# Performance work log

Hardware: AMD Instinct MI355X
Metric: run time of the kernel (lower is better)

## Reference

```python
import jax, jax.numpy as jnp
import numpy as np

B, S, E, HID, NH = 32, 512, 512, 512, 8
HD = E // NH  # head dim
A1, A2 = 1024, 1024  # architecture
EPS = 1e-5


def layer_norm(x, g, b):
    mu = jnp.mean(x, axis=-1, keepdims=True)
    var = jnp.mean(jnp.square(x - mu), axis=-1, keepdims=True)
    return (x - mu) * jax.lax.rsqrt(var + EPS) * g + b


def setup_inputs() -> dict:
    key = jax.random.key(0)
    ks = jax.random.split(key, 16)
    w = lambda k, shp: (jax.random.normal(k, shp, dtype=jnp.float32) * 0.02)
    return {
        'x': jax.random.normal(ks[0], (B, S, E), dtype=jnp.float32),
        'in_proj_w': w(ks[1], (3 * E, E)),
        'in_proj_b': jnp.zeros((3 * E,), jnp.float32),
        'out_proj_w': w(ks[2], (E, E)),
        'out_proj_b': jnp.zeros((E,), jnp.float32),
        'ln_g': jnp.ones((HID,), jnp.float32),
        'ln_b': jnp.zeros((HID,), jnp.float32),
        'w_ih': w(ks[3], (4 * HID, E)),
        'w_hh': w(ks[4], (4 * HID, HID)),
        'b_ih': jnp.zeros((4 * HID,), jnp.float32),
        'b_hh': jnp.zeros((4 * HID,), jnp.float32),
        'fc_w1': w(ks[5], (A1, HID)),
        'fc_b1': jnp.zeros((A1,), jnp.float32),
        'fc_w2': w(ks[6], (A2, A1)),
        'fc_b2': jnp.zeros((A2,), jnp.float32),
        'fc_wo': w(ks[7], (HID, A2)),
        'fc_bo': jnp.zeros((HID,), jnp.float32),
    }


def reference(x, in_proj_w, in_proj_b, out_proj_w, out_proj_b, ln_g, ln_b,
              w_ih, w_hh, b_ih, b_hh, fc_w1, fc_b1, fc_w2, fc_b2, fc_wo, fc_bo):
    # --- MultiheadAttention (self-attention, batch_first) ---
    qkv = x @ in_proj_w.T + in_proj_b            # [B,S,3E]
    q, k, v = jnp.split(qkv, 3, axis=-1)
    q = q.reshape(B, S, NH, HD)
    k = k.reshape(B, S, NH, HD)
    v = v.reshape(B, S, NH, HD)
    scores = jnp.einsum('bqhd,bkhd->bhqk', q, k) / np.float32(np.sqrt(HD))
    attn = jax.nn.softmax(scores, axis=-1)
    ctx = jnp.einsum('bhqk,bkhd->bqhd', attn, v).reshape(B, S, E)
    attn_out = ctx @ out_proj_w.T + out_proj_b
    attn_out = layer_norm(attn_out + x, ln_g, ln_b)  # [B,S,E]

    # --- LSTMCell unrolled over time via scan ---
    def step(carry, xt):
        hn, cn = carry
        gates = xt @ w_ih.T + b_ih + hn @ w_hh.T + b_hh  # [B,4H]
        i, f, g, o = jnp.split(gates, 4, axis=-1)
        i = jax.nn.sigmoid(i); f = jax.nn.sigmoid(f)
        g = jnp.tanh(g);       o = jax.nn.sigmoid(o)
        cn = f * cn + i * g
        hn = o * jnp.tanh(cn)
        return (hn, cn), hn

    h0 = jnp.zeros((B, HID), jnp.float32)
    c0 = jnp.zeros((B, HID), jnp.float32)
    (hn, cn), hs = jax.lax.scan(step, (h0, c0), attn_out.transpose(1, 0, 2))
    hs = hs.transpose(1, 0, 2)                   # [B,S,HID]

    # --- DeepNeuralNetwork MLP (applied pointwise over timesteps) ---
    h1 = jax.nn.relu(hs @ fc_w1.T + fc_b1)
    h2 = jax.nn.relu(h1 @ fc_w2.T + fc_b2)
    out = h2 @ fc_wo.T + fc_bo                   # [B,S,HID]

    out = layer_norm(out + attn_out, ln_g, ln_b)
    return out, (hn, cn)
```

## Files before the change

### kernel.cpp

```cpp
#include <hip/hip_runtime.h>

#define B_ 32
#define S_ 512
#define E_ 512
#define BS_ (B_*S_)

typedef __bf16 bf16x8 __attribute__((ext_vector_type(8)));
typedef float f32x4 __attribute__((ext_vector_type(4)));
typedef unsigned short u16x8 __attribute__((ext_vector_type(8)));

__device__ __forceinline__ unsigned short f2bf(float f){
  unsigned u = __float_as_uint(f);
  u += 0x7fffu + ((u>>16)&1u);
  return (unsigned short)(u>>16);
}
__device__ __forceinline__ float bf2f(unsigned short u){
  return __uint_as_float(((unsigned)u)<<16);
}
__device__ __forceinline__ float sigm(float x){ return 1.f/(1.f+__expf(-x)); }
__device__ __forceinline__ float tanh_f(float x){
  x = fminf(fmaxf(x,-15.f),15.f);
  float t=__expf(2.f*x); return (t-1.f)/(t+1.f);
}
__device__ __forceinline__ void gload_lds16(const void* g, void* l){
  __builtin_amdgcn_global_load_lds((const __attribute__((address_space(1))) unsigned int*)g,
                                   (__attribute__((address_space(3))) unsigned int*)l, 16, 0, 0);
}

__global__ void cast_bf16_k(const float* __restrict__ in, unsigned short* __restrict__ out, int n4){
  int i = blockIdx.x*256 + threadIdx.x;
  if (i < n4){
    const float4 v = *(const float4*)(in + (size_t)i*4);
    ushort4 o; o.x=f2bf(v.x); o.y=f2bf(v.y); o.z=f2bf(v.z); o.w=f2bf(v.w);
    *(ushort4*)(out + (size_t)i*4) = o;
  }
}
__global__ void addb_k(const float* __restrict__ a, const float* __restrict__ b, float* __restrict__ o, int n){
  int i = blockIdx.x*256 + threadIdx.x;
  if (i < n) o[i] = a[i] + b[i];
}
__global__ void sentinel_k(float* __restrict__ o){ o[0] = 1e9f; }

template<int OUTF , bool RELU>
__global__ __launch_bounds__(256) void gemm_bt(const unsigned short* __restrict__ A,
    const unsigned short* __restrict__ Bw, const float* __restrict__ bias,
    void* __restrict__ Cout, int M, int N, int K){
  __shared__ unsigned short As[128*32];
  __shared__ unsigned short Bs[128*32];
  const int tid = threadIdx.x, lane = tid&63, wid = tid>>6;
  const int bm = blockIdx.y, bn = blockIdx.x;
  const int wr = wid>>1, wc = wid&1;
  const int r = lane&15, kq = lane>>4;
  f32x4 acc[4][4] = {};
  const int nkt = K>>5;
  for (int kt=0; kt<nkt; ++kt){
#pragma unroll
    for (int i=0;i<2;++i){
      int cid = i*256 + tid;
      int row = cid>>2, kc = cid&3;
      int gcol = (kt<<5) + kc*8;
      gload_lds16(A  + (size_t)(bm*128+row)*K + gcol, (char*)As + (i*256 + wid*64)*16);
      gload_lds16(Bw + (size_t)(bn*128+row)*K + gcol, (char*)Bs + (i*256 + wid*64)*16);
    }
    __syncthreads();
    bf16x8 af[4], bfr[4];
#pragma unroll
    for (int i=0;i<4;++i){
      af[i]  = *(const bf16x8*)(As + (wr*64 + i*16 + r)*32 + kq*8);
      bfr[i] = *(const bf16x8*)(Bs + (wc*64 + i*16 + r)*32 + kq*8);
    }
#pragma unroll
    for (int i=0;i<4;++i)
#pragma unroll
      for (int j=0;j<4;++j)
        acc[i][j] = __builtin_amdgcn_mfma_f32_16x16x32_bf16(af[i], bfr[j], acc[i][j], 0,0,0);
    __syncthreads();
  }
#pragma unroll
  for (int j=0;j<4;++j){
    int n = bn*128 + wc*64 + j*16 + r;
    float bv = bias[n];
#pragma unroll
    for (int i=0;i<4;++i){
      int m0 = bm*128 + wr*64 + i*16 + kq*4;
#pragma unroll
      for (int jj=0;jj<4;++jj){
        float v = acc[i][j][jj] + bv;
        if (RELU) v = fmaxf(v, 0.f);
        size_t idx = (size_t)(m0+jj)*N + n;
        if (OUTF==0) ((unsigned short*)Cout)[idx] = f2bf(v);
        else         ((float*)Cout)[idx] = v;
      }
    }
  }
}

__global__ __launch_bounds__(256) void attn_k(const unsigned short* __restrict__ qkv,
                                              unsigned short* __restrict__ ctx){
  __shared__ unsigned short Qs[128*64];
  __shared__ unsigned short Ks[128*64];
  __shared__ unsigned short Vt[64*128];
  __shared__ unsigned short Ps[128*128];
  const int tid=threadIdx.x, lane=tid&63, wid=tid>>6;
  const int qt=blockIdx.x, bh=blockIdx.y, b=bh>>3, h=bh&7;
  const int r=lane&15, kq=lane>>4;
  const int q0=qt*128;
#pragma unroll
  for (int i=0;i<4;++i){
    int cid=i*256+tid; int row=cid>>3, dc=cid&7;
    u16x8 v = *(const u16x8*)(qkv + (size_t)(b*S_+q0+row)*1536 + h*64 + dc*8);
    int byte = (row*128 + dc*16) ^ ((row&7)<<4);
    *(u16x8*)((char*)Qs + byte) = v;
  }
  float m_run[2][4], l_run[2][4];
  f32x4 o_acc[2][4] = {};
#pragma unroll
  for (int a=0;a<2;++a)
#pragma unroll
    for (int j=0;j<4;++j){ m_run[a][j]=-1e30f; l_run[a][j]=0.f; }
  for (int kt=0; kt<4; ++kt){
#pragma unroll
    for (int i=0;i<4;++i){
      int cid=i*256+tid; int row=cid>>3, dc=cid&7;
      u16x8 v = *(const u16x8*)(qkv + (size_t)(b*S_+kt*128+row)*1536 + 512 + h*64 + dc*8);
      int byte = (row*128 + dc*16) ^ ((row&7)<<4);
      *(u16x8*)((char*)Ks + byte) = v;
    }
#pragma unroll
    for (int i=0;i<4;++i){
      int cid=i*256+tid; int sv=cid>>3, dc=cid&7;
      u16x8 v = *(const u16x8*)(qkv + (size_t)(b*S_+kt*128+sv)*1536 + 1024 + h*64 + dc*8);
#pragma unroll
      for (int e=0;e<8;++e){
        int d=dc*8+e;
        int byte = (d*256 + sv*2) ^ ((d&7)<<4);
        *(unsigned short*)((char*)Vt + byte) = (unsigned short)v[e];
      }
    }
    __syncthreads();
    f32x4 sa[2][8] = {};
#pragma unroll
    for (int dstep=0; dstep<2; ++dstep){
      int d0 = dstep*32 + kq*8;
      int q1 = wid*32 + r, q2 = wid*32 + 16 + r;
      bf16x8 a0 = *(const bf16x8*)((char*)Qs + ((q1*128 + d0*2) ^ ((q1&7)<<4)));
      bf16x8 a1 = *(const bf16x8*)((char*)Qs + ((q2*128 + d0*2) ^ ((q2&7)<<4)));
#pragma unroll
      for (int fk=0; fk<8; ++fk){
        int kc = fk*16 + r;
        bf16x8 bk = *(const bf16x8*)((char*)Ks + ((kc*128 + d0*2) ^ ((kc&7)<<4)));
        sa[0][fk] = __builtin_amdgcn_mfma_f32_16x16x32_bf16(a0, bk, sa[0][fk],0,0,0);
        sa[1][fk] = __builtin_amdgcn_mfma_f32_16x16x32_bf16(a1, bk, sa[1][fk],0,0,0);
      }
    }
#pragma unroll
    for (int fq=0; fq<2; ++fq){
#pragma unroll
      for (int j=0;j<4;++j){
        float mx = -1e30f;
#pragma unroll
        for (int fk=0;fk<8;++fk) mx = fmaxf(mx, sa[fq][fk][j]);
        mx *= 0.125f;
#pragma unroll
        for (int off=1; off<16; off<<=1) mx = fmaxf(mx, __shfl_xor(mx, off));
        float mn = fmaxf(m_run[fq][j], mx);
        float corr = __expf(m_run[fq][j] - mn);
        float ps = 0.f;
#pragma unroll
        for (int fk=0;fk<8;++fk){
          float p = __expf(sa[fq][fk][j]*0.125f - mn);
          sa[fq][fk][j] = p; ps += p;
        }
#pragma unroll
        for (int off=1; off<16; off<<=1) ps += __shfl_xor(ps, off);
        l_run[fq][j] = l_run[fq][j]*corr + ps;
        m_run[fq][j] = mn;
#pragma unroll
        for (int fd=0; fd<4; ++fd) o_acc[fq][fd][j] *= corr;
      }
    }
#pragma unroll
    for (int fq=0;fq<2;++fq)
#pragma unroll
      for (int fk=0;fk<8;++fk)
#pragma unroll
        for (int j=0;j<4;++j){
          int qr = wid*32 + fq*16 + kq*4 + j;
          int kc = fk*16 + r;
          int byte = (qr*256 + kc*2) ^ ((qr&7)<<4);
          *(unsigned short*)((char*)Ps + byte) = f2bf(sa[fq][fk][j]);
        }
#pragma unroll
    for (int kk=0;kk<4;++kk){
      int k0 = kk*32 + kq*8;
      bf16x8 pa[2];
#pragma unroll
      for (int fq=0;fq<2;++fq){
        int q = wid*32 + fq*16 + r;
        pa[fq] = *(const bf16x8*)((char*)Ps + ((q*256 + k0*2) ^ ((q&7)<<4)));
      }
#pragma unroll
      for (int fd=0; fd<4; ++fd){
        int d = fd*16 + r;
        bf16x8 bv = *(const bf16x8*)((char*)Vt + ((d*256 + k0*2) ^ ((d&7)<<4)));
        o_acc[0][fd] = __builtin_amdgcn_mfma_f32_16x16x32_bf16(pa[0], bv, o_acc[0][fd],0,0,0);
        o_acc[1][fd] = __builtin_amdgcn_mfma_f32_16x16x32_bf16(pa[1], bv, o_acc[1][fd],0,0,0);
      }
    }
    __syncthreads();
  }
#pragma unroll
  for (int fq=0;fq<2;++fq)
#pragma unroll
    for (int fd=0;fd<4;++fd)
#pragma unroll
      for (int j=0;j<4;++j){
        int qr = q0 + wid*32 + fq*16 + kq*4 + j;
        float v = o_acc[fq][fd][j] / l_run[fq][j];
        ctx[(size_t)(b*S_+qr)*512 + h*64 + fd*16 + r] = f2bf(v);
      }
}

template<bool DUAL>
__global__ __launch_bounds__(64) void ln_k(const float* __restrict__ raw, const float* __restrict__ res,
    const float* __restrict__ gam, const float* __restrict__ bet,
    float* __restrict__ outf, unsigned short* __restrict__ outb){
  const int row=blockIdx.x, lane=threadIdx.x;
  const size_t base=(size_t)row*512 + lane*8;
  float v[8];
  {
    float4 a0=*(const float4*)(raw+base), a1=*(const float4*)(raw+base+4);
    float4 b0=*(const float4*)(res+base), b1=*(const float4*)(res+base+4);
    v[0]=a0.x+b0.x; v[1]=a0.y+b0.y; v[2]=a0.z+b0.z; v[3]=a0.w+b0.w;
    v[4]=a1.x+b1.x; v[5]=a1.y+b1.y; v[6]=a1.z+b1.z; v[7]=a1.w+b1.w;
  }
  float s=0.f;
#pragma unroll
  for (int k=0;k<8;++k) s+=v[k];
#pragma unroll
  for (int off=1;off<64;off<<=1) s+=__shfl_xor(s,off);
  float mu=s*(1.f/512.f);
  float q=0.f;
#pragma unroll
  for (int k=0;k<8;++k){ float d=v[k]-mu; q+=d*d; }
#pragma unroll
  for (int off=1;off<64;off<<=1) q+=__shfl_xor(q,off);
  float rs=rsqrtf(q*(1.f/512.f)+1e-5f);
  float gv[8], bv[8];
  *(float4*)gv=*(const float4*)(gam+lane*8); *(float4*)(gv+4)=*(const float4*)(gam+lane*8+4);
  *(float4*)bv=*(const float4*)(bet+lane*8); *(float4*)(bv+4)=*(const float4*)(bet+lane*8+4);
  float y[8];
#pragma unroll
  for (int k=0;k<8;++k) y[k]=(v[k]-mu)*rs*gv[k]+bv[k];
  *(float4*)(outf+base)   = make_float4(y[0],y[1],y[2],y[3]);
  *(float4*)(outf+base+4) = make_float4(y[4],y[5],y[6],y[7]);
  if (DUAL){
    u16x8 ob;
#pragma unroll
    for (int k=0;k<8;++k) ob[k]=f2bf(y[k]);
    int row2 = ((row&511)<<5) | (row>>9);
    *(u16x8*)(outb + (size_t)row2*512 + lane*8)=ob;
  }
}

__global__ __launch_bounds__(256,1) void lstm_tag_k(
    const unsigned short* __restrict__ whh,
    const unsigned short* __restrict__ xpart,
    unsigned short* __restrict__ hs,
    float* __restrict__ hn_out, float* __restrict__ cn_out,
    unsigned* __restrict__ hxch)
{
  __shared__ unsigned short Wsl[64*512];
  __shared__ unsigned short Hb[32*512];
  const int tid=threadIdx.x, lane=tid&63, wid=tid>>6;
  const int wg=blockIdx.x;
  const int r=lane&15, kq=lane>>4;
  const int c=r, gate=c&3, uo=(wid<<2)+(c>>2), unit=wg*16+uo;
  const int colL=wid*16+c;
#pragma unroll
  for (int i=0;i<16;++i){
    int ch=i*256+tid; int lc=ch>>6, kc=ch&63;
    int uoo=((lc>>4)<<2)+((lc&15)>>2), gg=lc&3;
    u16x8 v = *(const u16x8*)(whh + (size_t)(gg*512 + wg*16 + uoo)*512 + kc*8);
    int byte=(lc*1024+kc*16)^((lc&7)<<4);
    *(u16x8*)((char*)Wsl+byte)=v;
  }
  {
    f32x4 z={0.f,0.f,0.f,0.f};
#pragma unroll
    for (int i=0;i<8;++i)
      *(f32x4*)((char*)Hb + (i*256+tid)*16) = z;
  }
  const int gb=tid>>3, gc=tid&7;
  float cst[8]={0,0,0,0,0,0,0,0}, hlast[8]={0,0,0,0,0,0,0,0};
  float xpc[8];
#pragma unroll
  for (int s=0;s<8;++s){
    int bb=(s>>2)*16 + kq*4 + (s&3);
    xpc[s]=bf2f(xpart[(size_t)bb*2048 + gate*512 + unit]);
  }
  __syncthreads();
  for (int t=0;t<512;++t){
    if (t){
      const unsigned* gp = hxch + (size_t)((t-1)&1)*16384 + gb*512 + gc*64;
      uint4 w0,w1,w2,w3,w4,w5,w6,w7,w8,w9,wa,wb,wc_,wd,we,wf;
      const unsigned tg=(unsigned)t;
      int it=0;
      for(;;){
        asm volatile(
          "global_load_dwordx4 %0, %16, off sc0 sc1\n\t"
          "global_load_dwordx4 %1, %16, off offset:16 sc0 sc1\n\t"
          "global_load_dwordx4 %2, %16, off offset:32 sc0 sc1\n\t"
          "global_load_dwordx4 %3, %16, off offset:48 sc0 sc1\n\t"
          "global_load_dwordx4 %4, %16, off offset:64 sc0 sc1\n\t"
          "global_load_dwordx4 %5, %16, off offset:80 sc0 sc1\n\t"
          "global_load_dwordx4 %6, %16, off offset:96 sc0 sc1\n\t"
          "global_load_dwordx4 %7, %16, off offset:112 sc0 sc1\n\t"
          "global_load_dwordx4 %8, %16, off offset:128 sc0 sc1\n\t"
          "global_load_dwordx4 %9, %16, off offset:144 sc0 sc1\n\t"
          "global_load_dwordx4 %10, %16, off offset:160 sc0 sc1\n\t"
          "global_load_dwordx4 %11, %16, off offset:176 sc0 sc1\n\t"
          "global_load_dwordx4 %12, %16, off offset:192 sc0 sc1\n\t"
          "global_load_dwordx4 %13, %16, off offset:208 sc0 sc1\n\t"
          "global_load_dwordx4 %14, %16, off offset:224 sc0 sc1\n\t"
          "global_load_dwordx4 %15, %16, off offset:240 sc0 sc1\n\t"
          "s_waitcnt vmcnt(0)"
          : "=&v"(w0),"=&v"(w1),"=&v"(w2),"=&v"(w3),"=&v"(w4),"=&v"(w5),"=&v"(w6),"=&v"(w7),
            "=&v"(w8),"=&v"(w9),"=&v"(wa),"=&v"(wb),"=&v"(wc_),"=&v"(wd),"=&v"(we),"=&v"(wf)
          : "v"(gp) : "memory");
        bool ok =
          ((w0.x&0xffffu)==tg)&((w0.y&0xffffu)==tg)&((w0.z&0xffffu)==tg)&((w0.w&0xffffu)==tg)&
          ((w1.x&0xffffu)==tg)&((w1.y&0xffffu)==tg)&((w1.z&0xffffu)==tg)&((w1.w&0xffffu)==tg)&
          ((w2.x&0xffffu)==tg)&((w2.y&0xffffu)==tg)&((w2.z&0xffffu)==tg)&((w2.w&0xffffu)==tg)&
          ((w3.x&0xffffu)==tg)&((w3.y&0xffffu)==tg)&((w3.z&0xffffu)==tg)&((w3.w&0xffffu)==tg)&
          ((w4.x&0xffffu)==tg)&((w4.y&0xffffu)==tg)&((w4.z&0xffffu)==tg)&((w4.w&0xffffu)==tg)&
          ((w5.x&0xffffu)==tg)&((w5.y&0xffffu)==tg)&((w5.z&0xffffu)==tg)&((w5.w&0xffffu)==tg)&
          ((w6.x&0xffffu)==tg)&((w6.y&0xffffu)==tg)&((w6.z&0xffffu)==tg)&((w6.w&0xffffu)==tg)&
          ((w7.x&0xffffu)==tg)&((w7.y&0xffffu)==tg)&((w7.z&0xffffu)==tg)&((w7.w&0xffffu)==tg)&
          ((w8.x&0xffffu)==tg)&((w8.y&0xffffu)==tg)&((w8.z&0xffffu)==tg)&((w8.w&0xffffu)==tg)&
          ((w9.x&0xffffu)==tg)&((w9.y&0xffffu)==tg)&((w9.z&0xffffu)==tg)&((w9.w&0xffffu)==tg)&
          ((wa.x&0xffffu)==tg)&((wa.y&0xffffu)==tg)&((wa.z&0xffffu)==tg)&((wa.w&0xffffu)==tg)&
          ((wb.x&0xffffu)==tg)&((wb.y&0xffffu)==tg)&((wb.z&0xffffu)==tg)&((wb.w&0xffffu)==tg)&
          ((wc_.x&0xffffu)==tg)&((wc_.y&0xffffu)==tg)&((wc_.z&0xffffu)==tg)&((wc_.w&0xffffu)==tg)&
          ((wd.x&0xffffu)==tg)&((wd.y&0xffffu)==tg)&((wd.z&0xffffu)==tg)&((wd.w&0xffffu)==tg)&
          ((we.x&0xffffu)==tg)&((we.y&0xffffu)==tg)&((we.z&0xffffu)==tg)&((we.w&0xffffu)==tg)&
          ((wf.x&0xffffu)==tg)&((wf.y&0xffffu)==tg)&((wf.z&0xffffu)==tg)&((wf.w&0xffffu)==tg);
        if (ok) break;
        if (++it>65536) break;
      }
      const int base = gb*1024 + gc*128;
      const int swz = (gb&7)<<4;
#define PACK2(WA,WB,G) { \
        uint4 p; \
        p.x=(WA.x>>16)|(WA.y&0xffff0000u); p.y=(WA.z>>16)|(WA.w&0xffff0000u); \
        p.z=(WB.x>>16)|(WB.y&0xffff0000u); p.w=(WB.z>>16)|(WB.w&0xffff0000u); \
        *(uint4*)((char*)Hb + ((base + (G)*16)^swz)) = p; }
      PACK2(w0,w1,0) PACK2(w2,w3,1) PACK2(w4,w5,2) PACK2(w6,w7,3)
      PACK2(w8,w9,4) PACK2(wa,wb,5) PACK2(wc_,wd,6) PACK2(we,wf,7)
#undef PACK2
    }
    __syncthreads();
    f32x4 acc[2];
    acc[0][0]=xpc[0]; acc[0][1]=xpc[1]; acc[0][2]=xpc[2]; acc[0][3]=xpc[3];
    acc[1][0]=xpc[4]; acc[1][1]=xpc[5]; acc[1][2]=xpc[6]; acc[1][3]=xpc[7];
#pragma unroll
    for (int ki=0;ki<16;++ki){
      int kb=ki*64+kq*16;
      bf16x8 a0=*(const bf16x8*)((char*)Hb+((r*1024+kb)^((r&7)<<4)));
      bf16x8 a1=*(const bf16x8*)((char*)Hb+(((16+r)*1024+kb)^((r&7)<<4)));
      bf16x8 bw=*(const bf16x8*)((char*)Wsl+((colL*1024+kb)^((colL&7)<<4)));
      acc[0]=__builtin_amdgcn_mfma_f32_16x16x32_bf16(a0,bw,acc[0],0,0,0);
      acc[1]=__builtin_amdgcn_mfma_f32_16x16x32_bf16(a1,bw,acc[1],0,0,0);
    }
    float xpn[8]={0,0,0,0,0,0,0,0};
    if (t<511){
#pragma unroll
      for (int s=0;s<8;++s){
        int bb=(s>>2)*16 + kq*4 + (s&3);
        xpn[s]=bf2f(xpart[(size_t)((t+1)*32+bb)*2048 + gate*512 + unit]);
      }
    }
    unsigned* pb = hxch + (size_t)(t&1)*16384;
#pragma unroll
    for (int s=0;s<8;++s){
      float v=acc[s>>2][s&3];
      float n1=__shfl_xor(v,1), n2=__shfl_xor(v,2), n3=__shfl_xor(v,3);
      if (gate==0){
        int bb=(s>>2)*16 + kq*4 + (s&3);
        float ig=sigm(v), fg=sigm(n1), gg2=tanh_f(n2), og=sigm(n3);
        float cn=fg*cst[s]+ig*gg2; cst[s]=cn;
        float hn=og*tanh_f(cn); hlast[s]=hn;
        unsigned h16=(unsigned)f2bf(hn);
        hs[((size_t)bb*512+t)*512 + unit]=(unsigned short)h16;
        unsigned word=(h16<<16)|(unsigned)(t+1);
        unsigned long long ad=(unsigned long long)(pb + bb*512 + unit);
        asm volatile("global_store_dword %0, %1, off sc0 sc1" :: "v"(ad), "v"(word) : "memory");
      }
    }
#pragma unroll
    for (int s=0;s<8;++s) xpc[s]=xpn[s];
    __syncthreads();
  }
  if (gate==0){
#pragma unroll
    for (int s=0;s<8;++s){
      int bb=(s>>2)*16 + kq*4 + (s&3);
      hn_out[(size_t)bb*512+unit]=hlast[s];
      cn_out[(size_t)bb*512+unit]=cst[s];
    }
  }
}

extern "C" void kernel_launch(void* const* d_in, const int* in_sizes, int n_in,
                              void* d_out, int out_size, void* d_ws, size_t ws_size,
                              hipStream_t stream) {
  const float* x          =(const float*)d_in[0];
  const float* in_proj_w  =(const float*)d_in[1];
  const float* in_proj_b  =(const float*)d_in[2];
  const float* out_proj_w =(const float*)d_in[3];
  const float* out_proj_b =(const float*)d_in[4];
  const float* ln_g       =(const float*)d_in[5];
  const float* ln_b       =(const float*)d_in[6];
  const float* w_ih       =(const float*)d_in[7];
  const float* w_hh       =(const float*)d_in[8];
  const float* b_ih       =(const float*)d_in[9];
  const float* b_hh       =(const float*)d_in[10];
  const float* fc_w1      =(const float*)d_in[11];
  const float* fc_b1      =(const float*)d_in[12];
  const float* fc_w2      =(const float*)d_in[13];
  const float* fc_b2      =(const float*)d_in[14];
  const float* fc_wo      =(const float*)d_in[15];
  const float* fc_bo      =(const float*)d_in[16];

  size_t off=0;
  auto A=[&](size_t b)->char*{ char* p=(char*)d_ws+off; off+=(b+255)&~(size_t)255; return p; };
  unsigned short* wqkv =(unsigned short*)A((size_t)1536*512*2);
  unsigned short* wout =(unsigned short*)A((size_t)512*512*2);
  unsigned short* wih  =(unsigned short*)A((size_t)2048*512*2);
  unsigned short* whh  =(unsigned short*)A((size_t)2048*512*2);
  unsigned short* w1   =(unsigned short*)A((size_t)1024*512*2);
  unsigned short* w2   =(unsigned short*)A((size_t)1024*1024*2);
  unsigned short* wo   =(unsigned short*)A((size_t)512*1024*2);
  float*          biasc=(float*)A(2048*4);
  unsigned*       hxch =(unsigned*)A((size_t)2*32*512*4);
  char* regA = A((size_t)BS_*512*2);
  char* regB = A((size_t)BS_*2048*2);
  char* regC = A((size_t)BS_*512*4);
  if (off > ws_size){ sentinel_k<<<1,1,0,stream>>>((float*)d_out); return; }

  unsigned short* xb        =(unsigned short*)regA;
  unsigned short* attn_outb =(unsigned short*)regA;
  unsigned short* hs        =(unsigned short*)regA;
  unsigned short* qkvb      =(unsigned short*)regB;
  unsigned short* ctxb      =(unsigned short*)(regB + (size_t)BS_*1536*2);
  unsigned short* xpart     =(unsigned short*)regB;
  unsigned short* h1b       =(unsigned short*)regB;
  unsigned short* h2b       =(unsigned short*)(regB + (size_t)BS_*1024*2);
  float*          attn_out  =(float*)regC;
  float* outp  =(float*)d_out;
  float* attn_raw = outp;
  float* out_raw  = outp;
  float* hn_out=outp + (size_t)BS_*512;
  float* cn_out=hn_out + (size_t)B_*512;

  auto cast=[&](const float* in, unsigned short* out, size_t n){
    int n4=(int)(n/4);
    cast_bf16_k<<<(n4+255)/256,256,0,stream>>>(in,out,n4);
  };
  cast(x, xb, (size_t)BS_*512);
  cast(in_proj_w, wqkv, (size_t)1536*512);
  cast(out_proj_w, wout, (size_t)512*512);
  cast(w_ih, wih, (size_t)2048*512);
  cast(w_hh, whh, (size_t)2048*512);
  cast(fc_w1, w1, (size_t)1024*512);
  cast(fc_w2, w2, (size_t)1024*1024);
  cast(fc_wo, wo, (size_t)512*1024);
  addb_k<<<8,256,0,stream>>>(b_ih,b_hh,biasc,2048);
  hipMemsetAsync(hxch,0,(size_t)2*32*512*4,stream);

  gemm_bt<0,false><<<dim3(12,128),256,0,stream>>>(xb,wqkv,in_proj_b,qkvb,BS_,1536,512);
  attn_k<<<dim3(4,256),256,0,stream>>>(qkvb,ctxb);
  gemm_bt<1,false><<<dim3(4,128),256,0,stream>>>(ctxb,wout,out_proj_b,attn_raw,BS_,512,512);
  ln_k<true><<<BS_,64,0,stream>>>(attn_raw,x,ln_g,ln_b,attn_out,attn_outb);
  gemm_bt<0,false><<<dim3(16,128),256,0,stream>>>(attn_outb,wih,biasc,xpart,BS_,2048,512);
  lstm_tag_k<<<32,256,0,stream>>>(whh,xpart,hs,hn_out,cn_out,hxch);
  gemm_bt<0,true><<<dim3(8,128),256,0,stream>>>(hs,w1,fc_b1,h1b,BS_,1024,512);
  gemm_bt<0,true><<<dim3(8,128),256,0,stream>>>(h1b,w2,fc_b2,h2b,BS_,1024,1024);
  gemm_bt<1,false><<<dim3(4,128),256,0,stream>>>(h2b,wo,fc_bo,out_raw,BS_,512,1024);
  ln_k<false><<<BS_,64,0,stream>>>(out_raw,attn_out,ln_g,ln_b,outp,nullptr);
}
```

Before: 4.225 ms.

## Replicate LSTM h-exchange per XCD, double-buffer LDS h, drop trailing barrier

Each block reads its XCD ID from a hardware register and polls a per-XCD replica of the hidden-state exchange buffer. Each producer now writes its tagged h word to all 8 replicas, so the consumer's polling reads can stay local instead of crossing dies. The LDS h buffer is double-buffered so the end-of-step __syncthreads can be removed. Gate activations are also computed once per lane before the shuffles rather than on the gate-0 lane. In exchange, producers issue eight times as many coherent stores, and the exchange buffer and its memset grow eightfold.

```diff
diff --git a/kernel.cpp b/kernel.cpp
--- a/kernel.cpp
+++ b/kernel.cpp
@@ -263,7 +263,7 @@
   }
 }
 
-__global__ __launch_bounds__(256,1) void lstm_tag_k(
+__global__ __launch_bounds__(256,1) void lstm_rep_k(
     const unsigned short* __restrict__ whh,
     const unsigned short* __restrict__ xpart,
     unsigned short* __restrict__ hs,
@@ -271,12 +271,13 @@
     unsigned* __restrict__ hxch)
 {
   __shared__ unsigned short Wsl[64*512];
-  __shared__ unsigned short Hb[32*512];
+  __shared__ unsigned short Hb[2*32*512];
   const int tid=threadIdx.x, lane=tid&63, wid=tid>>6;
   const int wg=blockIdx.x;
   const int r=lane&15, kq=lane>>4;
   const int c=r, gate=c&3, uo=(wid<<2)+(c>>2), unit=wg*16+uo;
   const int colL=wid*16+c;
+  const unsigned rep = __builtin_amdgcn_s_getreg((31u<<11)|20u) & 7u;
 #pragma unroll
   for (int i=0;i<16;++i){
     int ch=i*256+tid; int lc=ch>>6, kc=ch&63;
@@ -288,7 +289,7 @@
   {
     f32x4 z={0.f,0.f,0.f,0.f};
 #pragma unroll
-    for (int i=0;i<8;++i)
+    for (int i=0;i<16;++i)
       *(f32x4*)((char*)Hb + (i*256+tid)*16) = z;
   }
   const int gb=tid>>3, gc=tid&7;
@@ -301,8 +302,9 @@
   }
   __syncthreads();
   for (int t=0;t<512;++t){
+    const int cur32k = (t&1)*32768;
     if (t){
-      const unsigned* gp = hxch + (size_t)((t-1)&1)*16384 + gb*512 + gc*64;
+      const unsigned* gp = hxch + (size_t)rep*32768 + (size_t)((t-1)&1)*16384 + gb*512 + gc*64;
       uint4 w0,w1,w2,w3,w4,w5,w6,w7,w8,w9,wa,wb,wc_,wd,we,wf;
       const unsigned tg=(unsigned)t;
       int it=0;
@@ -348,26 +350,28 @@
         if (ok) break;
         if (++it>65536) break;
       }
-      const int base = gb*1024 + gc*128;
+      const int base = cur32k + gb*1024 + gc*128;
       const int swz = (gb&7)<<4;
 #define PACK2(WA,WB,G) { \
         uint4 p; \
         p.x=(WA.x>>16)|(WA.y&0xffff0000u); p.y=(WA.z>>16)|(WA.w&0xffff0000u); \
         p.z=(WB.x>>16)|(WB.y&0xffff0000u); p.w=(WB.z>>16)|(WB.w&0xffff0000u); \
-        *(uint4*)((char*)Hb + ((base + (G)*16)^swz)) = p; }
+        *(uint4*)((char*)Hb + cur32k + ((gb*1024 + gc*128 + (G)*16)^swz)) = p; }
       PACK2(w0,w1,0) PACK2(w2,w3,1) PACK2(w4,w5,2) PACK2(w6,w7,3)
       PACK2(w8,w9,4) PACK2(wa,wb,5) PACK2(wc_,wd,6) PACK2(we,wf,7)
 #undef PACK2
+      (void)base;
     }
     __syncthreads();
     f32x4 acc[2];
     acc[0][0]=xpc[0]; acc[0][1]=xpc[1]; acc[0][2]=xpc[2]; acc[0][3]=xpc[3];
     acc[1][0]=xpc[4]; acc[1][1]=xpc[5]; acc[1][2]=xpc[6]; acc[1][3]=xpc[7];
+    const char* hb = (const char*)Hb + cur32k;
 #pragma unroll
     for (int ki=0;ki<16;++ki){
       int kb=ki*64+kq*16;
-      bf16x8 a0=*(const bf16x8*)((char*)Hb+((r*1024+kb)^((r&7)<<4)));
-      bf16x8 a1=*(const bf16x8*)((char*)Hb+(((16+r)*1024+kb)^((r&7)<<4)));
+      bf16x8 a0=*(const bf16x8*)(hb+((r*1024+kb)^((r&7)<<4)));
+      bf16x8 a1=*(const bf16x8*)(hb+(((16+r)*1024+kb)^((r&7)<<4)));
       bf16x8 bw=*(const bf16x8*)((char*)Wsl+((colL*1024+kb)^((colL&7)<<4)));
       acc[0]=__builtin_amdgcn_mfma_f32_16x16x32_bf16(a0,bw,acc[0],0,0,0);
       acc[1]=__builtin_amdgcn_mfma_f32_16x16x32_bf16(a1,bw,acc[1],0,0,0);
@@ -384,22 +388,25 @@
 #pragma unroll
     for (int s=0;s<8;++s){
       float v=acc[s>>2][s&3];
-      float n1=__shfl_xor(v,1), n2=__shfl_xor(v,2), n3=__shfl_xor(v,3);
+      float act = (gate==2) ? tanh_f(v) : sigm(v);
+      float a1=__shfl_xor(act,1), a2=__shfl_xor(act,2), a3=__shfl_xor(act,3);
       if (gate==0){
         int bb=(s>>2)*16 + kq*4 + (s&3);
-        float ig=sigm(v), fg=sigm(n1), gg2=tanh_f(n2), og=sigm(n3);
-        float cn=fg*cst[s]+ig*gg2; cst[s]=cn;
-        float hn=og*tanh_f(cn); hlast[s]=hn;
+        float cn=a1*cst[s]+act*a2; cst[s]=cn;
+        float hn=a3*tanh_f(cn); hlast[s]=hn;
         unsigned h16=(unsigned)f2bf(hn);
         hs[((size_t)bb*512+t)*512 + unit]=(unsigned short)h16;
         unsigned word=(h16<<16)|(unsigned)(t+1);
-        unsigned long long ad=(unsigned long long)(pb + bb*512 + unit);
-        asm volatile("global_store_dword %0, %1, off sc0 sc1" :: "v"(ad), "v"(word) : "memory");
+        unsigned* wp = pb + bb*512 + unit;
+#pragma unroll
+        for (int rr=0; rr<8; ++rr){
+          asm volatile("global_store_dword %0, %1, off sc0 sc1"
+                       :: "v"((unsigned long long)(wp + (size_t)rr*32768)), "v"(word) : "memory");
+        }
       }
     }
 #pragma unroll
     for (int s=0;s<8;++s) xpc[s]=xpn[s];
-    __syncthreads();
   }
   if (gate==0){
 #pragma unroll
@@ -442,7 +449,7 @@
   unsigned short* w2   =(unsigned short*)A((size_t)1024*1024*2);
   unsigned short* wo   =(unsigned short*)A((size_t)512*1024*2);
   float*          biasc=(float*)A(2048*4);
-  unsigned*       hxch =(unsigned*)A((size_t)2*32*512*4);
+  unsigned*       hxch =(unsigned*)A((size_t)8*2*32*512*4);
   char* regA = A((size_t)BS_*512*2);
   char* regB = A((size_t)BS_*2048*2);
   char* regC = A((size_t)BS_*512*4);
@@ -476,14 +483,14 @@
   cast(fc_w2, w2, (size_t)1024*1024);
   cast(fc_wo, wo, (size_t)512*1024);
   addb_k<<<8,256,0,stream>>>(b_ih,b_hh,biasc,2048);
-  hipMemsetAsync(hxch,0,(size_t)2*32*512*4,stream);
+  hipMemsetAsync(hxch,0,(size_t)8*2*32*512*4,stream);
 
   gemm_bt<0,false><<<dim3(12,128),256,0,stream>>>(xb,wqkv,in_proj_b,qkvb,BS_,1536,512);
   attn_k<<<dim3(4,256),256,0,stream>>>(qkvb,ctxb);
   gemm_bt<1,false><<<dim3(4,128),256,0,stream>>>(ctxb,wout,out_proj_b,attn_raw,BS_,512,512);
   ln_k<true><<<BS_,64,0,stream>>>(attn_raw,x,ln_g,ln_b,attn_out,attn_outb);
   gemm_bt<0,false><<<dim3(16,128),256,0,stream>>>(attn_outb,wih,biasc,xpart,BS_,2048,512);
-  lstm_tag_k<<<32,256,0,stream>>>(whh,xpart,hs,hn_out,cn_out,hxch);
+  lstm_rep_k<<<32,256,0,stream>>>(whh,xpart,hs,hn_out,cn_out,hxch);
   gemm_bt<0,true><<<dim3(8,128),256,0,stream>>>(hs,w1,fc_b1,h1b,BS_,1024,512);
   gemm_bt<0,true><<<dim3(8,128),256,0,stream>>>(h1b,w2,fc_b2,h2b,BS_,1024,1024);
   gemm_bt<1,false><<<dim3(4,128),256,0,stream>>>(h2b,wo,fc_bo,out_raw,BS_,512,1024);
```

After: 5.405 ms. +27.9%, slower.
